# Kernel optimization log

Measured on AMD Instinct MI355X. Metric: run time of the kernel, lower is better.

Reference implementation:

```python
import jax, jax.numpy as jnp
import numpy as np

DMODEL = 1024
DK = 64
DHEAD = 16
DEPTH = DK * DHEAD
N, LQ, L = 2, 2048, 2048


def setup_inputs() -> dict:
    key = jax.random.key(0)
    ks = jax.random.split(key, 12)
    s = 1.0 / np.sqrt(DMODEL)
    inp = {
        'x': jax.random.normal(ks[0], (N, LQ, DMODEL), jnp.float32),
        'y': jax.random.normal(ks[1], (N, L, DMODEL), jnp.float32),
        'mask': jnp.tril(jnp.ones((LQ, L), dtype=bool)),  # causal
        'Wq': jax.random.normal(ks[2], (DMODEL, DEPTH), jnp.float32) * s,
        'bq': jnp.zeros((DEPTH,), jnp.float32),
        'Wk': jax.random.normal(ks[3], (DMODEL, DEPTH), jnp.float32) * s,
        'bk': jnp.zeros((DEPTH,), jnp.float32),
        'Wv': jax.random.normal(ks[4], (DMODEL, DEPTH), jnp.float32) * s,
        'bv': jnp.zeros((DEPTH,), jnp.float32),
        'Wo': jax.random.normal(ks[5], (DEPTH, DMODEL), jnp.float32) * (1.0 / np.sqrt(DEPTH)),
        'bo': jnp.zeros((DMODEL,), jnp.float32),
    }
    return inp


def reference(x, y, mask, Wq, bq, Wk, bk, Wv, bv, Wo, bo):
    fac = 1.0 / np.sqrt(DK)
    q = (x @ Wq + bq).reshape(N, LQ, DHEAD, DK).transpose(0, 2, 1, 3)  # N,H,Lq,dk
    k = (y @ Wk + bk).reshape(N, L, DHEAD, DK).transpose(0, 2, 1, 3)   # N,H,L,dk
    v = (y @ Wv + bv).reshape(N, L, DHEAD, DK).transpose(0, 2, 1, 3)   # N,H,L,dk
    scores = jnp.einsum('bhqd,bhkd->bhqk', q, k) * fac                 # N,H,Lq,L
    scores = jnp.where(mask, scores, -1e9)  # mask broadcasts over N,H
    attn = jax.nn.softmax(scores, axis=-1)
    out = jnp.einsum('bhqk,bhkd->bhqd', attn, v)                        # N,H,Lq,dk
    out = out.transpose(0, 2, 1, 3).reshape(N, LQ, DEPTH)
    return out @ Wo + bo
```

## Files before the change

kernel.cpp:

```cpp
#include <hip/hip_runtime.h>
#include <hip/hip_bf16.h>

typedef __attribute__((ext_vector_type(8))) short short8;
typedef __attribute__((ext_vector_type(4))) float floatx4;

#define LQ 2048
#define DM 1024
#define NH 16
#define LOG2E 1.44269504088896f

typedef __attribute__((address_space(1))) void gas_t;
typedef __attribute__((address_space(3))) void las_t;

__device__ __forceinline__ void async16(const __hip_bfloat16* g, __hip_bfloat16* l) {
    __builtin_amdgcn_global_load_lds((gas_t*)g, (las_t*)l, 16, 0, 0);
}

__global__ __launch_bounds__(256) void prep_all(
    const float* __restrict__ x,  const float* __restrict__ y,
    const float* __restrict__ Wq, const float* __restrict__ Wk,
    const float* __restrict__ Wv, const float* __restrict__ Wo,
    __hip_bfloat16* __restrict__ xb,  __hip_bfloat16* __restrict__ yb,
    __hip_bfloat16* __restrict__ Wqt, __hip_bfloat16* __restrict__ Wkt,
    __hip_bfloat16* __restrict__ Wvt, __hip_bfloat16* __restrict__ Wot)
{
    __shared__ float tile[64][65];
    const int t  = threadIdx.x;
    const int bx = blockIdx.x;

    if (bx < 4096) {
        const float* in = (bx < 2048) ? x : y;
        __hip_bfloat16* out = (bx < 2048) ? xb : yb;
        const int i = ((bx & 2047) * 256 + t) * 8;
        float4 a0 = ((const float4*)(in + i))[0];
        float4 a1 = ((const float4*)(in + i))[1];
        union { __hip_bfloat16 h[8]; uint4 u; } pk;
        pk.h[0] = __float2bfloat16(a0.x); pk.h[1] = __float2bfloat16(a0.y);
        pk.h[2] = __float2bfloat16(a0.z); pk.h[3] = __float2bfloat16(a0.w);
        pk.h[4] = __float2bfloat16(a1.x); pk.h[5] = __float2bfloat16(a1.y);
        pk.h[6] = __float2bfloat16(a1.z); pk.h[7] = __float2bfloat16(a1.w);
        *(uint4*)(out + i) = pk.u;
        return;
    }

    const int r    = bx - 4096;
    const int wsel = r >> 8;
    const int tid  = r & 255;
    const int n0   = (tid & 15) * 64, k0 = (tid >> 4) * 64;
    const float* W = (wsel == 0) ? Wq : (wsel == 1) ? Wk : (wsel == 2) ? Wv : Wo;
    __hip_bfloat16* Wt = (wsel == 0) ? Wqt : (wsel == 1) ? Wkt : (wsel == 2) ? Wvt : Wot;

    const int rr0 = t >> 4, c4 = (t & 15) * 4;
#pragma unroll
    for (int rr = 0; rr < 64; rr += 16) {
        float4 v = *(const float4*)&W[(size_t)(k0 + rr0 + rr) * DM + n0 + c4];
        tile[rr0 + rr][c4 + 0] = v.x; tile[rr0 + rr][c4 + 1] = v.y;
        tile[rr0 + rr][c4 + 2] = v.z; tile[rr0 + rr][c4 + 3] = v.w;
    }
    __syncthreads();
    const int nr = t >> 2, kc = (t & 3) * 16;
    union { __hip_bfloat16 h[16]; uint4 u[2]; } pk;
#pragma unroll
    for (int i = 0; i < 16; ++i) pk.h[i] = __float2bfloat16(tile[kc + i][nr]);
    uint4* dst = (uint4*)&Wt[(size_t)(n0 + nr) * DM + k0 + kc];
    dst[0] = pk.u[0];
    dst[1] = pk.u[1];
}

__global__ __launch_bounds__(256) void gemm_qkv(
    const __hip_bfloat16* __restrict__ xb,
    const __hip_bfloat16* __restrict__ yb,
    const __hip_bfloat16* __restrict__ Bt,
    const float* __restrict__ bq, const float* __restrict__ bk,
    const float* __restrict__ bv,
    __hip_bfloat16* __restrict__ Qb, __hip_bfloat16* __restrict__ Kb,
    __hip_bfloat16* __restrict__ Vt,
    float qscl)
{
    constexpr int BM = 128, BN = 128, BK = 32, Kd = 1024;
    __shared__ __align__(16) __hip_bfloat16 As[2][BM * BK];
    __shared__ __align__(16) __hip_bfloat16 Bs[2][BN * BK];

    const int t    = threadIdx.x;
    const int w    = t >> 6;
    const int lane = t & 63;
    const int quad = lane >> 4;
    const int l16  = lane & 15;
    const int wm   = w & 1;
    const int wn   = w >> 1;

    const int f  = blockIdx.x;
    const int rx = f & 7;
    const int rr = f >> 3;
    const int bx = (rx & 1) * 12 + rr % 12;
    const int by = (rx >> 1) * 8 + rr / 12;
    const int m0 = by * BM;
    const int n0 = bx * BN;

    const int region = n0 >> 10;
    const int nl     = n0 & 1023;

    const __hip_bfloat16* A = (region == 0) ? xb : yb;

    const int lrow = lane >> 2;
    const int lcol = (lane & 3) * 8;

    floatx4 acc[4][4];
#pragma unroll
    for (int i = 0; i < 4; ++i)
#pragma unroll
        for (int j = 0; j < 4; ++j) acc[i][j] = (floatx4){0.f, 0.f, 0.f, 0.f};

    auto stage = [&](int k0, int buf) {
#pragma unroll
        for (int s = 0; s < 2; ++s) {
            const int seg = w * 2 + s;
            async16(A + (size_t)(m0 + seg * 16 + lrow) * Kd + k0 + lcol,
                    &As[buf][seg * 16 * BK]);
            async16(Bt + (size_t)(n0 + seg * 16 + lrow) * Kd + k0 + lcol,
                    &Bs[buf][seg * 16 * BK]);
        }
    };

    stage(0, 0);
    int cur = 0;
    for (int k0 = 0; k0 < Kd; k0 += BK) {
        __syncthreads();
        if (k0 + BK < Kd) stage(k0 + BK, cur ^ 1);

        short8 af[4], bf[4];
#pragma unroll
        for (int i = 0; i < 4; ++i)
            af[i] = *(const short8*)&As[cur][(wm * 64 + i * 16 + l16) * BK + quad * 8];
#pragma unroll
        for (int j = 0; j < 4; ++j)
            bf[j] = *(const short8*)&Bs[cur][(wn * 64 + j * 16 + l16) * BK + quad * 8];
#pragma unroll
        for (int i = 0; i < 4; ++i)
#pragma unroll
            for (int j = 0; j < 4; ++j)
                acc[i][j] = __builtin_amdgcn_mfma_f32_16x16x32_bf16(af[i], bf[j], acc[i][j], 0, 0, 0);
        cur ^= 1;
    }

    if (region < 2) {
        __hip_bfloat16* C    = (region == 0) ? Qb : Kb;
        const float*    bias = (region == 0) ? bq : bk;
        const float     scl  = (region == 0) ? qscl : 1.0f;
#pragma unroll
        for (int j = 0; j < 4; ++j) {
            const int col = nl + wn * 64 + j * 16 + l16;
            const float bvv = bias[col];
#pragma unroll
            for (int i = 0; i < 4; ++i) {
#pragma unroll
                for (int r = 0; r < 4; ++r) {
                    const int row = m0 + wm * 64 + i * 16 + quad * 4 + r;
                    C[(size_t)row * 1024 + col] = __float2bfloat16((acc[i][j][r] + bvv) * scl);
                }
            }
        }
    } else {
#pragma unroll
        for (int j = 0; j < 4; ++j) {
            const int col = nl + wn * 64 + j * 16 + l16;
            const float bvv = bv[col];
#pragma unroll
            for (int i = 0; i < 4; ++i) {
                const int row0 = m0 + wm * 64 + i * 16 + quad * 4;
                union { __hip_bfloat16 h4[4]; uint2 u; } pk;
#pragma unroll
                for (int r = 0; r < 4; ++r)
                    pk.h4[r] = __float2bfloat16(acc[i][j][r] + bvv);
                *(uint2*)&Vt[((size_t)((row0 >> 11) * 1024 + col)) * 2048 + (row0 & 2047)] = pk.u;
            }
        }
    }
}

__global__ __launch_bounds__(256) void gemm_o(
    const __hip_bfloat16* __restrict__ A,
    const __hip_bfloat16* __restrict__ Bt,
    const float* __restrict__ bias,
    float* __restrict__ C,
    int M)
{
    constexpr int BM = 64, BN = 128, BK = 32, Kd = 1024;
    __shared__ __align__(16) __hip_bfloat16 As[2][BM * BK];
    __shared__ __align__(16) __hip_bfloat16 Bs[2][BN * BK];

    const int t    = threadIdx.x;
    const int w    = t >> 6;
    const int lane = t & 63;
    const int quad = lane >> 4;
    const int l16  = lane & 15;
    const int wm   = w & 1;
    const int wn   = w >> 1;

    const int f  = blockIdx.x;
    const int rx = f & 7;
    const int rr = f >> 3;
    const int bx = (rx & 1) * 4 + (rr & 3);
    const int by = (rx >> 1) * 16 + (rr >> 2);
    const int m0 = by * BM;
    const int n0 = bx * BN;

    const int lrow = lane >> 2;
    const int lcol = (lane & 3) * 8;

    floatx4 acc[2][4];
#pragma unroll
    for (int i = 0; i < 2; ++i)
#pragma unroll
        for (int j = 0; j < 4; ++j) acc[i][j] = (floatx4){0.f, 0.f, 0.f, 0.f};

    auto stage = [&](int k0, int buf) {
#pragma unroll
        for (int s = 0; s < 3; ++s) {
            const int seg = w * 3 + s;
            if (seg < 4) {
                async16(A + (size_t)(m0 + seg * 16 + lrow) * Kd + k0 + lcol,
                        &As[buf][seg * 16 * BK]);
            } else {
                const int bs = seg - 4;
                async16(Bt + (size_t)(n0 + bs * 16 + lrow) * Kd + k0 + lcol,
                        &Bs[buf][bs * 16 * BK]);
            }
        }
    };

    stage(0, 0);
    int cur = 0;
    for (int k0 = 0; k0 < Kd; k0 += BK) {
        __syncthreads();
        if (k0 + BK < Kd) stage(k0 + BK, cur ^ 1);

        short8 af[2], bf[4];
#pragma unroll
        for (int i = 0; i < 2; ++i)
            af[i] = *(const short8*)&As[cur][(wm * 32 + i * 16 + l16) * BK + quad * 8];
#pragma unroll
        for (int j = 0; j < 4; ++j)
            bf[j] = *(const short8*)&Bs[cur][(wn * 64 + j * 16 + l16) * BK + quad * 8];
#pragma unroll
        for (int i = 0; i < 2; ++i)
#pragma unroll
            for (int j = 0; j < 4; ++j)
                acc[i][j] = __builtin_amdgcn_mfma_f32_16x16x32_bf16(af[i], bf[j], acc[i][j], 0, 0, 0);
        cur ^= 1;
    }

#pragma unroll
    for (int j = 0; j < 4; ++j) {
        const int col = n0 + wn * 64 + j * 16 + l16;
        const float bvf = bias[col];
#pragma unroll
        for (int i = 0; i < 2; ++i) {
#pragma unroll
            for (int r = 0; r < 4; ++r) {
                const int row = m0 + wm * 32 + i * 16 + quad * 4 + r;
                C[(size_t)row * 1024 + col] = acc[i][j][r] + bvf;
            }
        }
    }
}

template <bool A_IS_F32, bool OUT_F32, bool TRANSV = false>
__global__ __launch_bounds__(256) void gemm64(
    const void* __restrict__ Av,
    const float* __restrict__ B,
    const float* __restrict__ bias,
    void* __restrict__ Cv,
    int M, int N, int K, float scale)
{
    __shared__ __align__(16) __hip_bfloat16 As[64][40];
    __shared__ __align__(16) __hip_bfloat16 Bs[64][40];

    const int t    = threadIdx.x;
    const int wave = t >> 6;
    const int lane = t & 63;
    const int quad = lane >> 4;
    const int l16  = lane & 15;
    const int m0   = blockIdx.y * 64;
    const int n0   = blockIdx.x * 64;

    floatx4 acc[4];
#pragma unroll
    for (int i = 0; i < 4; ++i) acc[i] = (floatx4){0.f, 0.f, 0.f, 0.f};

    const int arow = t >> 2, acol = (t & 3) * 8;
    const int bkk  = t >> 3, bnn  = (t & 7) * 8;

    for (int k0 = 0; k0 < K; k0 += 32) {
        if constexpr (A_IS_F32) {
            const float* A = (const float*)Av;
            const float* ap = A + (size_t)(m0 + arow) * K + k0 + acol;
            float4 a0 = ((const float4*)ap)[0];
            float4 a1 = ((const float4*)ap)[1];
            union { __hip_bfloat16 h[8]; short8 s; } up;
            up.h[0] = __float2bfloat16(a0.x); up.h[1] = __float2bfloat16(a0.y);
            up.h[2] = __float2bfloat16(a0.z); up.h[3] = __float2bfloat16(a0.w);
            up.h[4] = __float2bfloat16(a1.x); up.h[5] = __float2bfloat16(a1.y);
            up.h[6] = __float2bfloat16(a1.z); up.h[7] = __float2bfloat16(a1.w);
            *(short8*)(&As[arow][acol]) = up.s;
        } else {
            const __hip_bfloat16* A = (const __hip_bfloat16*)Av;
            uint4 av = *(const uint4*)(A + (size_t)(m0 + arow) * K + k0 + acol);
            *(uint4*)(&As[arow][acol]) = av;
        }
        {
            const float* bp = B + (size_t)(k0 + bkk) * N + n0 + bnn;
            float4 b0 = ((const float4*)bp)[0];
            float4 b1 = ((const float4*)bp)[1];
            Bs[bnn + 0][bkk] = __float2bfloat16(b0.x);
            Bs[bnn + 1][bkk] = __float2bfloat16(b0.y);
            Bs[bnn + 2][bkk] = __float2bfloat16(b0.z);
            Bs[bnn + 3][bkk] = __float2bfloat16(b0.w);
            Bs[bnn + 4][bkk] = __float2bfloat16(b1.x);
            Bs[bnn + 5][bkk] = __float2bfloat16(b1.y);
            Bs[bnn + 6][bkk] = __float2bfloat16(b1.z);
            Bs[bnn + 7][bkk] = __float2bfloat16(b1.w);
        }
        __syncthreads();

        short8 afrag = *(const short8*)(&As[wave * 16 + l16][quad * 8]);
#pragma unroll
        for (int nt = 0; nt < 4; ++nt) {
            short8 bfrag = *(const short8*)(&Bs[nt * 16 + l16][quad * 8]);
            acc[nt] = __builtin_amdgcn_mfma_f32_16x16x32_bf16(afrag, bfrag, acc[nt], 0, 0, 0);
        }
        __syncthreads();
    }

#pragma unroll
    for (int nt = 0; nt < 4; ++nt) {
        const int col = n0 + nt * 16 + l16;
        const float bvf = bias[col];
        if constexpr (TRANSV) {
            const int row0 = m0 + wave * 16 + quad * 4;
            union { __hip_bfloat16 h4[4]; uint2 u; } pk;
#pragma unroll
            for (int r = 0; r < 4; ++r)
                pk.h4[r] = __float2bfloat16(acc[nt][r] + bvf);
            *(uint2*)&((__hip_bfloat16*)Cv)[((size_t)((row0 >> 11) * 1024 + col)) * 2048 + (row0 & 2047)] = pk.u;
        } else {
#pragma unroll
            for (int r = 0; r < 4; ++r) {
                const int row = m0 + wave * 16 + quad * 4 + r;
                const float v = (acc[nt][r] + bvf) * scale;
                if constexpr (OUT_F32) ((float*)Cv)[(size_t)row * N + col] = v;
                else ((__hip_bfloat16*)Cv)[(size_t)row * N + col] = __float2bfloat16(v);
            }
        }
    }
}

#define PP 72

__global__ __launch_bounds__(256, 2) void attn_mfma8(
    const __hip_bfloat16* __restrict__ Q,
    const __hip_bfloat16* __restrict__ K,
    const __hip_bfloat16* __restrict__ Vt,
    __hip_bfloat16* __restrict__ O)
{
    __shared__ __align__(16) __hip_bfloat16 KtS[3][64 * 64];
    __shared__ __align__(16) __hip_bfloat16 VtS[3][64 * 64];
    __shared__ __align__(16) __hip_bfloat16 PsQ[128 * PP];

    const int t    = threadIdx.x;
    const int w    = t >> 6;
    const int lane = t & 63;
    const int quad = lane >> 4;
    const int l16  = lane & 15;

    const int f  = blockIdx.x;
    const int p  = (f & 7) * 4 + ((f >> 3) >> 4);
    const int qx = (f >> 3) & 15;
    const int h  = p & 15;
    const int b  = p >> 4;
    const int q0 = qx * 128;

    const size_t rowbase = (size_t)b * LQ;
    const int    hcol    = h * 64;
    const size_t vbase   = (size_t)(b * NH + h) * 64 * LQ;

    const int r8 = l16 & 7;

    auto stage = [&](int j0n, int buf) {
#pragma unroll
        for (int rnd = 0; rnd < 2; ++rnd) {
            const int c   = rnd * 256 + t;
            const int row = c >> 3;
            const int ch  = (c & 7) ^ (row & 7);
            async16(K + (rowbase + j0n + row) * DM + hcol + ch * 8,
                    &KtS[buf][c * 8]);
            async16(Vt + vbase + (size_t)row * LQ + j0n + ch * 8,
                    &VtS[buf][c * 8]);
        }
    };

    {
        const int qrow = t >> 1, qseg = (t & 1) * 32;
        const uint4* src = (const uint4*)(Q + (rowbase + q0 + qrow) * DM + hcol + qseg);
        uint4* dst = (uint4*)&PsQ[qrow * PP + qseg];
        dst[0] = src[0]; dst[1] = src[1]; dst[2] = src[2]; dst[3] = src[3];
    }
    stage(0, 0);
    stage(64, 1);

    short8 qf[2][2];
#pragma unroll
    for (int g = 0; g < 2; ++g)
#pragma unroll
        for (int hh = 0; hh < 2; ++hh)
            qf[g][hh] = *(const short8*)&PsQ[(w * 32 + g * 16 + l16) * PP + hh * 32 + quad * 8];

    __hip_bfloat16* Pw = &PsQ[(w * 32) * PP];

    float l_i[2] = {0.f, 0.f};
    floatx4 o[2][4];
#pragma unroll
    for (int g = 0; g < 2; ++g)
#pragma unroll
        for (int i = 0; i < 4; ++i) o[g][i] = (floatx4){0.f, 0.f, 0.f, 0.f};

    const int wq_lo  = q0 + w * 32;
    const int wq_hi  = wq_lo + 31;
    const int ntiles = 2 * qx + 2;

    int cur = 0;
    for (int jt = 0; jt < ntiles; ++jt) {
        const int j0 = jt * 64;

        if (jt + 2 < ntiles) stage(j0 + 128, (cur + 2 >= 3) ? cur - 1 : cur + 2);

        const int rem = (ntiles - 1 - jt > 2) ? 2 : (ntiles - 1 - jt);
        if (rem >= 2)      asm volatile("s_waitcnt vmcnt(8)" ::: "memory");
        else if (rem == 1) asm volatile("s_waitcnt vmcnt(4)" ::: "memory");
        else               asm volatile("s_waitcnt vmcnt(0)" ::: "memory");
        __builtin_amdgcn_sched_barrier(0);
        __builtin_amdgcn_s_barrier();

        if (j0 <= wq_hi) {
            const bool bnd = (j0 + 63 > wq_lo);
#pragma unroll
            for (int jc = 0; jc < 4; ++jc) {
                const __hip_bfloat16* kr = &KtS[cur][(jc * 16 + l16) * 64];
                short8 ak0 = *(const short8*)&kr[((quad    ) ^ r8) * 8];
                short8 ak1 = *(const short8*)&kr[((quad + 4) ^ r8) * 8];
#pragma unroll
                for (int g = 0; g < 2; ++g) {
                    floatx4 z = (floatx4){0.f, 0.f, 0.f, 0.f};
                    z = __builtin_amdgcn_mfma_f32_16x16x32_bf16(ak0, qf[g][0], z, 0, 0, 0);
                    z = __builtin_amdgcn_mfma_f32_16x16x32_bf16(ak1, qf[g][1], z, 0, 0, 0);
                    if (bnd) {
                        const int qg = wq_lo + g * 16 + l16;
#pragma unroll
                        for (int r = 0; r < 4; ++r) {
                            const int j = j0 + jc * 16 + quad * 4 + r;
                            if (j > qg) z[r] = -1e30f;
                        }
                    }
                    union { __hip_bfloat16 h4[4]; uint2 u; } pk;
#pragma unroll
                    for (int r = 0; r < 4; ++r) {
                        const float e = __builtin_amdgcn_exp2f(z[r]);
                        l_i[g] += e;
                        pk.h4[r] = __float2bfloat16(e);
                    }
                    *(uint2*)&Pw[(g * 16 + l16) * PP + jc * 16 + quad * 4] = pk.u;
                }
            }
            short8 pa[2][2];
#pragma unroll
            for (int g = 0; g < 2; ++g) {
                pa[g][0] = *(const short8*)&Pw[(g * 16 + l16) * PP + quad * 8];
                pa[g][1] = *(const short8*)&Pw[(g * 16 + l16) * PP + 32 + quad * 8];
            }
#pragma unroll
            for (int subf = 0; subf < 4; ++subf) {
                const __hip_bfloat16* vr = &VtS[cur][(subf * 16 + l16) * 64];
                short8 vb0 = *(const short8*)&vr[((quad    ) ^ r8) * 8];
                short8 vb1 = *(const short8*)&vr[((quad + 4) ^ r8) * 8];
#pragma unroll
                for (int g = 0; g < 2; ++g) {
                    o[g][subf] = __builtin_amdgcn_mfma_f32_16x16x32_bf16(pa[g][0], vb0, o[g][subf], 0, 0, 0);
                    o[g][subf] = __builtin_amdgcn_mfma_f32_16x16x32_bf16(pa[g][1], vb1, o[g][subf], 0, 0, 0);
                }
            }
        }
        cur = (cur + 1 >= 3) ? 0 : cur + 1;
    }

#pragma unroll
    for (int g = 0; g < 2; ++g) {
        l_i[g] += __shfl_xor(l_i[g], 16);
        l_i[g] += __shfl_xor(l_i[g], 32);
#pragma unroll
        for (int r = 0; r < 4; ++r) {
            const float linv = 1.0f / __shfl(l_i[g], quad * 4 + r);
            const size_t row = rowbase + q0 + w * 32 + g * 16 + quad * 4 + r;
#pragma unroll
            for (int subf = 0; subf < 4; ++subf)
                O[row * DM + hcol + subf * 16 + l16] = __float2bfloat16(o[g][subf][r] * linv);
        }
    }
}

extern "C" void kernel_launch(void* const* d_in, const int* in_sizes, int n_in,
                              void* d_out, int out_size, void* d_ws, size_t ws_size,
                              hipStream_t stream)
{
    (void)in_sizes; (void)n_in; (void)out_size;

    const float* x  = (const float*)d_in[0];
    const float* y  = (const float*)d_in[1];
    const float* Wq = (const float*)d_in[3];
    const float* bq = (const float*)d_in[4];
    const float* Wk = (const float*)d_in[5];
    const float* bk = (const float*)d_in[6];
    const float* Wv = (const float*)d_in[7];
    const float* bv = (const float*)d_in[8];
    const float* Wo = (const float*)d_in[9];
    const float* bo = (const float*)d_in[10];

    const size_t NTOK = (size_t)2 * LQ * DM;
    const size_t MM   = (size_t)DM * DM;
    const int    M    = 2 * LQ;
    const float  QSCL = 0.125f * LOG2E;

    __hip_bfloat16* Qb  = (__hip_bfloat16*)d_ws;
    __hip_bfloat16* Kb  = Qb + NTOK;
    __hip_bfloat16* Vtb = Kb + NTOK;
    __hip_bfloat16* Ab  = Vtb + NTOK;

    const size_t need = (4 * NTOK + 2 * NTOK + 4 * MM) * sizeof(__hip_bfloat16);
    const dim3 agrid(512, 1, 1);

    if (ws_size >= need) {
        __hip_bfloat16* xb  = Ab + NTOK;
        __hip_bfloat16* yb  = xb + NTOK;
        __hip_bfloat16* Wqt = yb + NTOK;
        __hip_bfloat16* Wkt = Wqt + MM;
        __hip_bfloat16* Wvt = Wkt + MM;
        __hip_bfloat16* Wot = Wvt + MM;
        (void)Wkt; (void)Wvt;

        prep_all<<<5120, 256, 0, stream>>>(x, y, Wq, Wk, Wv, Wo,
                                           xb, yb, Wqt, Wkt, Wvt, Wot);

        gemm_qkv<<<768, 256, 0, stream>>>(xb, yb, Wqt, bq, bk, bv, Qb, Kb, Vtb, QSCL);
        attn_mfma8<<<agrid, 256, 0, stream>>>(Qb, Kb, Vtb, Ab);
        gemm_o<<<512, 256, 0, stream>>>(Ab, Wot, bo, (float*)d_out, M);
    } else {
        const dim3 gblk(DM / 64, M / 64);
        gemm64<true,  false><<<gblk, 256, 0, stream>>>(x, Wq, bq, Qb, M, DM, DM, QSCL);
        gemm64<true,  false><<<gblk, 256, 0, stream>>>(y, Wk, bk, Kb, M, DM, DM, 1.0f);
        gemm64<true,  false, true><<<gblk, 256, 0, stream>>>(y, Wv, bv, Vtb, M, DM, DM, 1.0f);
        attn_mfma8<<<agrid, 256, 0, stream>>>(Qb, Kb, Vtb, Ab);
        gemm64<false, true ><<<gblk, 256, 0, stream>>>(Ab, Wo, bo, (float*)d_out, M, DM, DM, 1.0f);
    }
}
```

Measured before the change: 234.6 us.

## Triple-buffer GEMM K-loops and move attention prefetch after barrier

Both projection GEMMs go from double to triple buffering of their LDS tiles. They issue two stages ahead and use explicit vmcnt waits plus s_barrier in place of __syncthreads, so global loads overlap more compute. The attention kernel now issues its next-tile prefetch after the barrier with a simpler wait count. This keeps the in-flight load count consistent and means a single barrier per iteration is enough to guard buffer reuse. LDS usage per GEMM block grows by half, which may reduce occupancy.

```diff
diff --git a/kernel.cpp b/kernel.cpp
--- a/kernel.cpp
+++ b/kernel.cpp
@@ -77,9 +77,9 @@
     __hip_bfloat16* __restrict__ Vt,
     float qscl)
 {
-    constexpr int BM = 128, BN = 128, BK = 32, Kd = 1024;
-    __shared__ __align__(16) __hip_bfloat16 As[2][BM * BK];
-    __shared__ __align__(16) __hip_bfloat16 Bs[2][BN * BK];
+    constexpr int BM = 128, BN = 128, BK = 32, Kd = 1024, NIT = Kd / BK;
+    __shared__ __align__(16) __hip_bfloat16 As[3][BM * BK];
+    __shared__ __align__(16) __hip_bfloat16 Bs[3][BN * BK];
 
     const int t    = threadIdx.x;
     const int w    = t >> 6;
@@ -123,24 +123,28 @@
     };
 
     stage(0, 0);
+    stage(BK, 1);
     int cur = 0;
-    for (int k0 = 0; k0 < Kd; k0 += BK) {
-        __syncthreads();
-        if (k0 + BK < Kd) stage(k0 + BK, cur ^ 1);
+    for (int i = 0; i < NIT; ++i) {
+        if (i < NIT - 1) asm volatile("s_waitcnt vmcnt(4)" ::: "memory");
+        else             asm volatile("s_waitcnt vmcnt(0)" ::: "memory");
+        __builtin_amdgcn_sched_barrier(0);
+        __builtin_amdgcn_s_barrier();
+        if (i + 2 < NIT) stage((i + 2) * BK, (cur + 2 >= 3) ? cur - 1 : cur + 2);
 
         short8 af[4], bf[4];
 #pragma unroll
-        for (int i = 0; i < 4; ++i)
-            af[i] = *(const short8*)&As[cur][(wm * 64 + i * 16 + l16) * BK + quad * 8];
+        for (int ii = 0; ii < 4; ++ii)
+            af[ii] = *(const short8*)&As[cur][(wm * 64 + ii * 16 + l16) * BK + quad * 8];
 #pragma unroll
         for (int j = 0; j < 4; ++j)
             bf[j] = *(const short8*)&Bs[cur][(wn * 64 + j * 16 + l16) * BK + quad * 8];
 #pragma unroll
-        for (int i = 0; i < 4; ++i)
+        for (int ii = 0; ii < 4; ++ii)
 #pragma unroll
             for (int j = 0; j < 4; ++j)
-                acc[i][j] = __builtin_amdgcn_mfma_f32_16x16x32_bf16(af[i], bf[j], acc[i][j], 0, 0, 0);
-        cur ^= 1;
+                acc[ii][j] = __builtin_amdgcn_mfma_f32_16x16x32_bf16(af[ii], bf[j], acc[ii][j], 0, 0, 0);
+        cur = (cur + 1 >= 3) ? 0 : cur + 1;
     }
 
     if (region < 2) {
@@ -185,9 +189,9 @@
     float* __restrict__ C,
     int M)
 {
-    constexpr int BM = 64, BN = 128, BK = 32, Kd = 1024;
-    __shared__ __align__(16) __hip_bfloat16 As[2][BM * BK];
-    __shared__ __align__(16) __hip_bfloat16 Bs[2][BN * BK];
+    constexpr int BM = 64, BN = 128, BK = 32, Kd = 1024, NIT = Kd / BK;
+    __shared__ __align__(16) __hip_bfloat16 As[3][BM * BK];
+    __shared__ __align__(16) __hip_bfloat16 Bs[3][BN * BK];
 
     const int t    = threadIdx.x;
     const int w    = t >> 6;
@@ -230,24 +234,28 @@
     };
 
     stage(0, 0);
+    stage(BK, 1);
     int cur = 0;
-    for (int k0 = 0; k0 < Kd; k0 += BK) {
-        __syncthreads();
-        if (k0 + BK < Kd) stage(k0 + BK, cur ^ 1);
+    for (int i = 0; i < NIT; ++i) {
+        if (i < NIT - 1) asm volatile("s_waitcnt vmcnt(3)" ::: "memory");
+        else             asm volatile("s_waitcnt vmcnt(0)" ::: "memory");
+        __builtin_amdgcn_sched_barrier(0);
+        __builtin_amdgcn_s_barrier();
+        if (i + 2 < NIT) stage((i + 2) * BK, (cur + 2 >= 3) ? cur - 1 : cur + 2);
 
         short8 af[2], bf[4];
 #pragma unroll
-        for (int i = 0; i < 2; ++i)
-            af[i] = *(const short8*)&As[cur][(wm * 32 + i * 16 + l16) * BK + quad * 8];
+        for (int ii = 0; ii < 2; ++ii)
+            af[ii] = *(const short8*)&As[cur][(wm * 32 + ii * 16 + l16) * BK + quad * 8];
 #pragma unroll
         for (int j = 0; j < 4; ++j)
             bf[j] = *(const short8*)&Bs[cur][(wn * 64 + j * 16 + l16) * BK + quad * 8];
 #pragma unroll
-        for (int i = 0; i < 2; ++i)
+        for (int ii = 0; ii < 2; ++ii)
 #pragma unroll
             for (int j = 0; j < 4; ++j)
-                acc[i][j] = __builtin_amdgcn_mfma_f32_16x16x32_bf16(af[i], bf[j], acc[i][j], 0, 0, 0);
-        cur ^= 1;
+                acc[ii][j] = __builtin_amdgcn_mfma_f32_16x16x32_bf16(af[ii], bf[j], acc[ii][j], 0, 0, 0);
+        cur = (cur + 1 >= 3) ? 0 : cur + 1;
     }
 
 #pragma unroll
@@ -357,7 +365,7 @@
 
 #define PP 72
 
-__global__ __launch_bounds__(256, 2) void attn_mfma8(
+__global__ __launch_bounds__(256, 2) void attn_mfma9(
     const __hip_bfloat16* __restrict__ Q,
     const __hip_bfloat16* __restrict__ K,
     const __hip_bfloat16* __restrict__ Vt,
@@ -432,14 +440,11 @@
     for (int jt = 0; jt < ntiles; ++jt) {
         const int j0 = jt * 64;
 
-        if (jt + 2 < ntiles) stage(j0 + 128, (cur + 2 >= 3) ? cur - 1 : cur + 2);
-
-        const int rem = (ntiles - 1 - jt > 2) ? 2 : (ntiles - 1 - jt);
-        if (rem >= 2)      asm volatile("s_waitcnt vmcnt(8)" ::: "memory");
-        else if (rem == 1) asm volatile("s_waitcnt vmcnt(4)" ::: "memory");
-        else               asm volatile("s_waitcnt vmcnt(0)" ::: "memory");
+        if (jt < ntiles - 1) asm volatile("s_waitcnt vmcnt(4)" ::: "memory");
+        else                 asm volatile("s_waitcnt vmcnt(0)" ::: "memory");
         __builtin_amdgcn_sched_barrier(0);
         __builtin_amdgcn_s_barrier();
+        if (jt + 2 < ntiles) stage(j0 + 128, (cur + 2 >= 3) ? cur - 1 : cur + 2);
 
         if (j0 <= wq_hi) {
             const bool bnd = (j0 + 63 > wq_lo);
@@ -550,14 +555,14 @@
                                            xb, yb, Wqt, Wkt, Wvt, Wot);
 
         gemm_qkv<<<768, 256, 0, stream>>>(xb, yb, Wqt, bq, bk, bv, Qb, Kb, Vtb, QSCL);
-        attn_mfma8<<<agrid, 256, 0, stream>>>(Qb, Kb, Vtb, Ab);
+        attn_mfma9<<<agrid, 256, 0, stream>>>(Qb, Kb, Vtb, Ab);
         gemm_o<<<512, 256, 0, stream>>>(Ab, Wot, bo, (float*)d_out, M);
     } else {
         const dim3 gblk(DM / 64, M / 64);
         gemm64<true,  false><<<gblk, 256, 0, stream>>>(x, Wq, bq, Qb, M, DM, DM, QSCL);
         gemm64<true,  false><<<gblk, 256, 0, stream>>>(y, Wk, bk, Kb, M, DM, DM, 1.0f);
         gemm64<true,  false, true><<<gblk, 256, 0, stream>>>(y, Wv, bv, Vtb, M, DM, DM, 1.0f);
-        attn_mfma8<<<agrid, 256, 0, stream>>>(Qb, Kb, Vtb, Ab);
+        attn_mfma9<<<agrid, 256, 0, stream>>>(Qb, Kb, Vtb, Ab);
         gemm64<false, true ><<<gblk, 256, 0, stream>>>(Ab, Wo, bo, (float*)d_out, M, DM, DM, 1.0f);
     }
 }
```

Measured after the change: 231.0 us. No clear change (-1.6%).
